# Kernel optimization log

Measured on AMD Instinct MI355X. Metric: run time of the kernel, lower is better.

## Reference

```python
import jax, jax.numpy as jnp
import numpy as np

D_MODEL = 768
N_HEAD = 12
BATCH = 2
SEQ = 2048
MASK_FILL = -100000.0


def setup_inputs() -> dict:
    key = jax.random.key(0)
    ks = jax.random.split(key, 10)
    s = 1.0 / np.sqrt(D_MODEL)
    inp = {
        "xEnc": jax.random.normal(ks[0], (BATCH, SEQ, D_MODEL), jnp.float32),
        "xDec": jax.random.normal(ks[1], (BATCH, SEQ, D_MODEL), jnp.float32),
        # causal mask: True where attention is disallowed (j > i)
        "mask": (jnp.arange(SEQ)[None, :] > jnp.arange(SEQ)[:, None])[None, None, :, :],
        "wQ": jax.random.uniform(ks[2], (D_MODEL, D_MODEL), jnp.float32, -s, s),
        "bQ": jax.random.uniform(ks[3], (D_MODEL,), jnp.float32, -s, s),
        "wK": jax.random.uniform(ks[4], (D_MODEL, D_MODEL), jnp.float32, -s, s),
        "bK": jax.random.uniform(ks[5], (D_MODEL,), jnp.float32, -s, s),
        "wV": jax.random.uniform(ks[6], (D_MODEL, D_MODEL), jnp.float32, -s, s),
        "bV": jax.random.uniform(ks[7], (D_MODEL,), jnp.float32, -s, s),
        "wOut": jax.random.uniform(ks[8], (D_MODEL, D_MODEL), jnp.float32, -s, s),
        "bOut": jax.random.uniform(ks[9], (D_MODEL,), jnp.float32, -s, s),
    }
    return inp


def reference(xEnc, xDec, mask, wQ, bQ, wK, bK, wV, bV, wOut, bOut):
    B, S, D = xEnc.shape
    H = N_HEAD
    Dh = D // H
    # torch Linear: y = x @ W.T + b
    Q = xDec @ wQ.T + bQ
    K = xEnc @ wK.T + bK
    V = xEnc @ wV.T + bV
    Q = Q.reshape(B, S, H, Dh).transpose(0, 2, 1, 3)  # [B,H,S,Dh]
    K = K.reshape(B, S, H, Dh).transpose(0, 2, 1, 3)
    V = V.reshape(B, S, H, Dh).transpose(0, 2, 1, 3)
    score = jnp.einsum("bhqd,bhkd->bhqk", Q, K) / jnp.sqrt(jnp.float32(Dh))
    score = jnp.where(mask, MASK_FILL, score)
    attn = jax.nn.softmax(score, axis=-1)
    ctx = jnp.einsum("bhqk,bhkd->bhqd", attn, V)  # [B,H,S,Dh]
    ctx = ctx.transpose(0, 2, 1, 3).reshape(B, S, D)
    return ctx @ wOut.T + bOut
```

## Files before the change

kernel.cpp:

```cpp
#include <hip/hip_runtime.h>
#include <stdint.h>
#include <stddef.h>

#define DMODEL 768
#define NHEAD 12
#define SEQLEN 2048
#define NBATCH 2
#define DH 64
#define MTOT (NBATCH*SEQLEN)

typedef short s16x4 __attribute__((ext_vector_type(4)));
typedef short s16x8 __attribute__((ext_vector_type(8)));
typedef float f32x4 __attribute__((ext_vector_type(4)));

#define XDECB_OFF 0u
#define XENCB_OFF 3145728u
#define WQB_OFF   6291456u
#define WKB_OFF   6881280u
#define WVB_OFF   7471104u
#define WOUTB_OFF 8060928u
#define QB_OFF    8650752u
#define KB_OFF    11796480u
#define VT_OFF    14942208u
#define CTXB_OFF  18087936u

#define QSCALE 0.18033688011112042f

static __device__ __forceinline__ unsigned short f2bf(float f) {
  union { float f; unsigned int u; } v; v.f = f;
  unsigned int r = v.u + 0x7fffu + ((v.u >> 16) & 1u);
  return (unsigned short)(r >> 16);
}

static __device__ __forceinline__ unsigned int pack2bf(float f0, float f1) {
  union { float f; unsigned int u; } a, b; a.f = f0; b.f = f1;
  return __builtin_amdgcn_perm(b.u + 0x8000u, a.u + 0x8000u, 0x07060302u);
}

#if __has_builtin(__builtin_amdgcn_exp2f)
#define EXP2(x) __builtin_amdgcn_exp2f(x)
#else
#define EXP2(x) exp2f(x)
#endif

static __device__ __forceinline__ f32x4 mfma16(s16x4 a, s16x4 b, f32x4 c) {
  return __builtin_amdgcn_mfma_f32_16x16x16bf16_1k(a, b, c, 0, 0, 0);
}
static __device__ __forceinline__ f32x4 mfma32(s16x8 a, s16x8 b, f32x4 c) {
  return __builtin_amdgcn_mfma_f32_16x16x32_bf16(a, b, c, 0, 0, 0);
}

typedef __attribute__((address_space(3))) unsigned int lds_u32_t;
typedef const __attribute__((address_space(1))) unsigned int glb_u32_t;
static __device__ __forceinline__ void gl_lds16(const unsigned short* g,
                                                unsigned short* l) {
  __builtin_amdgcn_global_load_lds((glb_u32_t*)g, (lds_u32_t*)l, 16, 0, 0);
}

__global__ __launch_bounds__(256) void cvt_kernel(
    const float* __restrict__ xDec, const float* __restrict__ xEnc,
    const float* __restrict__ wQ, const float* __restrict__ wK,
    const float* __restrict__ wV, const float* __restrict__ wOut,
    unsigned short* __restrict__ ws)
{
  const int seg = blockIdx.y;
  const float* src;
  unsigned int n4, off;
  switch (seg) {
    case 0:  src = xDec; n4 = 786432; off = XDECB_OFF; break;
    case 1:  src = xEnc; n4 = 786432; off = XENCB_OFF; break;
    case 2:  src = wQ;   n4 = 147456; off = WQB_OFF;   break;
    case 3:  src = wK;   n4 = 147456; off = WKB_OFF;   break;
    case 4:  src = wV;   n4 = 147456; off = WVB_OFF;   break;
    default: src = wOut; n4 = 147456; off = WOUTB_OFF; break;
  }
  unsigned short* d = ws + off;
  const unsigned int stride = gridDim.x * blockDim.x;
  for (unsigned int i = blockIdx.x * blockDim.x + threadIdx.x; i < n4; i += stride) {
    const float4 v = ((const float4*)src)[i];
    s16x4 p;
    p[0] = (short)f2bf(v.x); p[1] = (short)f2bf(v.y);
    p[2] = (short)f2bf(v.z); p[3] = (short)f2bf(v.w);
    ((s16x4*)d)[i] = p;
  }
}

#define BK 64
#define NKT (DMODEL / BK)

__global__ __launch_bounds__(256, 3) void qkv_gemm(
    const unsigned short* __restrict__ xDecB, const unsigned short* __restrict__ xEncB,
    const unsigned short* __restrict__ wQB, const unsigned short* __restrict__ wKB,
    const unsigned short* __restrict__ wVB,
    const float* __restrict__ bQ, const float* __restrict__ bK, const float* __restrict__ bV,
    unsigned short* __restrict__ Qb, unsigned short* __restrict__ Kb,
    unsigned short* __restrict__ Vt)
{
  const int z = blockIdx.z;
  const unsigned short* __restrict__ A = (z == 0) ? xDecB : xEncB;
  const unsigned short* __restrict__ B = (z == 0) ? wQB : ((z == 1) ? wKB : wVB);
  const float* __restrict__ bias = (z == 0) ? bQ : ((z == 1) ? bK : bV);

  __shared__ unsigned short lA[3][64 * BK];
  __shared__ unsigned short lB[3][64 * BK];

  const int tid  = threadIdx.x;
  const int lane = tid & 63;
  const int wid  = tid >> 6;
  const int ln   = lane & 15;
  const int qd   = lane >> 4;
  const int m0 = blockIdx.x * 64;
  const int n0 = blockIdx.y * 64;
  const int wm = (wid & 1) * 32;
  const int wn = (wid >> 1) * 32;

  int srow[2], scol[2];
  #pragma unroll
  for (int c = 0; c < 2; ++c) {
    const int s = c * 256 + wid * 64 + lane;
    srow[c] = s >> 3;
    scol[c] = (((s & 7) ^ ((s >> 3) & 7)) * 8);
  }

  auto stage = [&](int buf, int k0) {
    #pragma unroll
    for (int c = 0; c < 2; ++c) {
      const int ldsoff = (c * 256 + wid * 64) * 8;
      gl_lds16(A + (size_t)(m0 + srow[c]) * DMODEL + k0 + scol[c], &lA[buf][ldsoff]);
      gl_lds16(B + (size_t)(n0 + srow[c]) * DMODEL + k0 + scol[c], &lB[buf][ldsoff]);
    }
  };

  f32x4 acc[2][2] = {};

  stage(0, 0);
  stage(1, BK);

  auto step = [&](int t, int bc, int bs) {
    if (t == NKT - 1) asm volatile("s_waitcnt vmcnt(0)" ::: "memory");
    else              asm volatile("s_waitcnt vmcnt(4)" ::: "memory");
    __builtin_amdgcn_s_barrier();
    __builtin_amdgcn_sched_barrier(0);
    if (t + 2 < NKT) stage(bs, (t + 2) * BK);
    #pragma unroll
    for (int kc = 0; kc < 2; ++kc) {
      s16x8 af[2], bfr[2];
      #pragma unroll
      for (int i = 0; i < 2; ++i) {
        const int r = wm + i * 16 + ln;
        af[i] = *(const s16x8*)&lA[bc][r * 64 + (((kc * 4 + qd) ^ (r & 7)) * 8)];
      }
      #pragma unroll
      for (int j = 0; j < 2; ++j) {
        const int r = wn + j * 16 + ln;
        bfr[j] = *(const s16x8*)&lB[bc][r * 64 + (((kc * 4 + qd) ^ (r & 7)) * 8)];
      }
      #pragma unroll
      for (int i = 0; i < 2; ++i)
        #pragma unroll
        for (int j = 0; j < 2; ++j)
          acc[i][j] = mfma32(af[i], bfr[j], acc[i][j]);
    }
  };

  for (int tb = 0; tb < NKT; tb += 3) {
    step(tb + 0, 0, 2);
    step(tb + 1, 1, 0);
    step(tb + 2, 2, 1);
  }

  #pragma unroll
  for (int j = 0; j < 2; ++j) {
    const int n_g = n0 + wn + j * 16 + ln;
    const float bv = bias[n_g];
    const int h    = n_g >> 6;
    const int dcol = n_g & 63;
    #pragma unroll
    for (int i = 0; i < 2; ++i) {
      #pragma unroll
      for (int r = 0; r < 4; ++r) {
        const int m_g  = m0 + wm + i * 16 + qd * 4 + r;
        const int bb   = m_g >> 11;
        const int srow2 = m_g & 2047;
        const float val = acc[i][j][r] + bv;
        if (z == 0)
          Qb[((size_t)((bb * NHEAD + h) * SEQLEN + srow2)) * DH + dcol] = f2bf(val * QSCALE);
        else if (z == 1)
          Kb[((size_t)((bb * NHEAD + h) * SEQLEN + srow2)) * DH + dcol] = f2bf(val);
        else
          Vt[((size_t)((bb * NHEAD + h) * DH + dcol)) * SEQLEN + srow2] = f2bf(val);
      }
    }
  }
}

__global__ __launch_bounds__(256, 3) void out_gemm(
    const unsigned short* __restrict__ ctx, const unsigned short* __restrict__ wOutB,
    const float* __restrict__ bOut, float* __restrict__ out)
{
  __shared__ unsigned short lA[3][64 * BK];
  __shared__ unsigned short lB[3][64 * BK];

  const int tid  = threadIdx.x;
  const int lane = tid & 63;
  const int wid  = tid >> 6;
  const int ln   = lane & 15;
  const int qd   = lane >> 4;
  const int m0 = blockIdx.x * 64;
  const int n0 = blockIdx.y * 64;
  const int wm = (wid & 1) * 32;
  const int wn = (wid >> 1) * 32;

  int srow[2], scol[2];
  #pragma unroll
  for (int c = 0; c < 2; ++c) {
    const int s = c * 256 + wid * 64 + lane;
    srow[c] = s >> 3;
    scol[c] = (((s & 7) ^ ((s >> 3) & 7)) * 8);
  }

  auto stage = [&](int buf, int k0) {
    #pragma unroll
    for (int c = 0; c < 2; ++c) {
      const int ldsoff = (c * 256 + wid * 64) * 8;
      gl_lds16(ctx + (size_t)(m0 + srow[c]) * DMODEL + k0 + scol[c], &lA[buf][ldsoff]);
      gl_lds16(wOutB + (size_t)(n0 + srow[c]) * DMODEL + k0 + scol[c], &lB[buf][ldsoff]);
    }
  };

  f32x4 acc[2][2] = {};

  stage(0, 0);
  stage(1, BK);

  auto step = [&](int t, int bc, int bs) {
    if (t == NKT - 1) asm volatile("s_waitcnt vmcnt(0)" ::: "memory");
    else              asm volatile("s_waitcnt vmcnt(4)" ::: "memory");
    __builtin_amdgcn_s_barrier();
    __builtin_amdgcn_sched_barrier(0);
    if (t + 2 < NKT) stage(bs, (t + 2) * BK);
    #pragma unroll
    for (int kc = 0; kc < 2; ++kc) {
      s16x8 af[2], bfr[2];
      #pragma unroll
      for (int i = 0; i < 2; ++i) {
        const int r = wm + i * 16 + ln;
        af[i] = *(const s16x8*)&lA[bc][r * 64 + (((kc * 4 + qd) ^ (r & 7)) * 8)];
      }
      #pragma unroll
      for (int j = 0; j < 2; ++j) {
        const int r = wn + j * 16 + ln;
        bfr[j] = *(const s16x8*)&lB[bc][r * 64 + (((kc * 4 + qd) ^ (r & 7)) * 8)];
      }
      #pragma unroll
      for (int i = 0; i < 2; ++i)
        #pragma unroll
        for (int j = 0; j < 2; ++j)
          acc[i][j] = mfma32(af[i], bfr[j], acc[i][j]);
    }
  };

  for (int tb = 0; tb < NKT; tb += 3) {
    step(tb + 0, 0, 2);
    step(tb + 1, 1, 0);
    step(tb + 2, 2, 1);
  }

  #pragma unroll
  for (int j = 0; j < 2; ++j) {
    const int n_g = n0 + wn + j * 16 + ln;
    const float bv = bOut[n_g];
    #pragma unroll
    for (int i = 0; i < 2; ++i) {
      #pragma unroll
      for (int r = 0; r < 4; ++r) {
        const int m_g = m0 + wm + i * 16 + qd * 4 + r;
        out[(size_t)m_g * DMODEL + n_g] = acc[i][j][r] + bv;
      }
    }
  }
}

#define KVT 128
#define LKP 72
#define LVP 136

__global__ __launch_bounds__(256, 3) void attn_kernel(
    const unsigned short* __restrict__ Qb, const unsigned short* __restrict__ Kb,
    const unsigned short* __restrict__ Vt, unsigned short* __restrict__ ctx,
    float* __restrict__ pout0, float* __restrict__ pout1,
    float* __restrict__ lpart)
{
  __shared__ unsigned short lK[KVT * LKP];
  __shared__ unsigned short lV[DH * LVP];

  const int tid  = threadIdx.x;
  const int lane = tid & 63;
  const int wid  = tid >> 6;
  const int ln   = lane & 15;
  const int qd   = lane >> 4;

  const int ord  = blockIdx.x;
  const int xcd  = ord & 7;
  const int slot = ord >> 3;
  const int bh   = xcd * 3 + (slot >> 5);
  const int p    = slot & 31;

  const bool isA = p < 16;
  const int i  = isA ? p : (p - 16);
  const int Ti = (i + 2) >> 1;

  const unsigned short* Kbase = Kb + (size_t)bh * SEQLEN * DH;
  const unsigned short* Vbase = Vt + (size_t)bh * DH * SEQLEN;
  const int bb = bh / NHEAD;
  const int h  = bh % NHEAD;

  auto run = [&](int q0, int t0, int nt, int mode) {
    const int q_lane = q0 + wid * 16 + ln;
    s16x8 qf[2];
    {
      const unsigned short* Qrow = Qb + ((size_t)bh * SEQLEN + q_lane) * DH;
      qf[0] = *(const s16x8*)(Qrow + qd * 8);
      qf[1] = *(const s16x8*)(Qrow + 32 + qd * 8);
    }
    float l_run = 0.0f;
    f32x4 o_acc[4] = {};

    s16x8 rK[4], rV[4];
    auto load_kv = [&](int kv0) {
      #pragma unroll
      for (int c = 0; c < 4; ++c) {
        const int f = tid + c * 256;
        rK[c] = *(const s16x8*)(Kbase + (size_t)(kv0 + (f >> 3)) * DH + (f & 7) * 8);
      }
      #pragma unroll
      for (int c = 0; c < 4; ++c) {
        const int f = tid + c * 256;
        rV[c] = *(const s16x8*)(Vbase + (size_t)(f >> 4) * SEQLEN + kv0 + (f & 15) * 8);
      }
    };

    load_kv(t0 * KVT);
    for (int t = t0; t < t0 + nt; ++t) {
      const int kv0 = t * KVT;
      #pragma unroll
      for (int c = 0; c < 4; ++c) {
        const int f = tid + c * 256;
        *(s16x8*)&lK[(f >> 3) * LKP + (f & 7) * 8] = rK[c];
      }
      #pragma unroll
      for (int c = 0; c < 4; ++c) {
        const int f = tid + c * 256;
        *(s16x8*)&lV[(f >> 4) * LVP + (f & 15) * 8] = rV[c];
      }
      __syncthreads();
      if (t + 1 < t0 + nt) load_kv(kv0 + KVT);

      f32x4 s_acc[8] = {};
      #pragma unroll
      for (int kc = 0; kc < 2; ++kc) {
        #pragma unroll
        for (int t8 = 0; t8 < 8; ++t8) {
          const s16x8 a = *(const s16x8*)&lK[(t8 * 16 + ln) * LKP + kc * 32 + qd * 8];
          s_acc[t8] = mfma32(a, qf[kc], s_acc[t8]);
        }
      }

      if (kv0 + KVT > q0) {
        #pragma unroll
        for (int t8 = 0; t8 < 8; ++t8) {
          #pragma unroll
          for (int r = 0; r < 4; ++r) {
            const int kv = kv0 + t8 * 16 + qd * 4 + r;
            s_acc[t8][r] = (kv > q_lane) ? -1e30f : s_acc[t8][r];
          }
        }
      }

      s16x4 pf[8];
      #pragma unroll
      for (int t8 = 0; t8 < 8; ++t8) {
        const float p0 = EXP2(s_acc[t8][0]);
        const float p1 = EXP2(s_acc[t8][1]);
        const float p2 = EXP2(s_acc[t8][2]);
        const float p3 = EXP2(s_acc[t8][3]);
        l_run += (p0 + p1) + (p2 + p3);
        union { unsigned int u[2]; s16x4 v; } pk;
        pk.u[0] = pack2bf(p0, p1);
        pk.u[1] = pack2bf(p2, p3);
        pf[t8] = pk.v;
      }

      #pragma unroll
      for (int t8 = 0; t8 < 8; ++t8) {
        #pragma unroll
        for (int j = 0; j < 4; ++j) {
          const s16x4 b = *(const s16x4*)&lV[(j * 16 + ln) * LVP + t8 * 16 + qd * 4];
          o_acc[j] = mfma16(pf[t8], b, o_acc[j]);
        }
      }
      __syncthreads();
    }

    l_run += __shfl_xor(l_run, 16);
    l_run += __shfl_xor(l_run, 32);

    if (mode == 0) {
      #pragma unroll
      for (int r = 0; r < 4; ++r) {
        const float lr  = __shfl(l_run, qd * 4 + r);
        const float inv = 1.0f / lr;
        const int q_g = q0 + wid * 16 + qd * 4 + r;
        unsigned short* dst = ctx + ((size_t)bb * SEQLEN + q_g) * DMODEL + h * DH;
        #pragma unroll
        for (int j = 0; j < 4; ++j)
          dst[j * 16 + ln] = f2bf(o_acc[j][r] * inv);
      }
    } else {
      float* PO = (mode == 1) ? pout1 : pout0;
      float* LO = lpart + ((mode == 1) ? (24 * 1024) : 0);
      const int qbase = q0 - 1024 + wid * 16;
      if (lane < 16)
        LO[bh * 1024 + qbase + lane] = l_run;
      #pragma unroll
      for (int j = 0; j < 4; ++j)
        #pragma unroll
        for (int r = 0; r < 4; ++r)
          PO[((size_t)bh * 1024 + qbase + qd * 4 + r) * 64 + j * 16 + ln] =
              o_acc[j][r];
    }
  };

  if (isA) {
    run(i * 64, 0, Ti, 0);
    run((31 - i) * 64, 0, 9 - Ti, 1);
  } else {
    run((31 - i) * 64, 9 - Ti, 8, 2);
  }
}

__global__ __launch_bounds__(256) void norm_kernel(
    const float* __restrict__ pout0, const float* __restrict__ pout1,
    const float* __restrict__ lpart, unsigned short* __restrict__ ctx)
{
  const int e4  = blockIdx.x * 256 + threadIdx.x;
  const int d4  = e4 & 15;
  const int row = e4 >> 4;
  const int bh  = row >> 10;
  const int qr  = row & 1023;
  const float l = lpart[row] + lpart[24 * 1024 + row];
  const float inv = 1.0f / l;
  const float4 a = ((const float4*)pout0)[e4];
  const float4 b = ((const float4*)pout1)[e4];
  const int bb = bh / NHEAD;
  const int h  = bh % NHEAD;
  unsigned short* dst =
      ctx + ((size_t)bb * SEQLEN + 1024 + qr) * DMODEL + h * DH + d4 * 4;
  s16x4 o;
  o[0] = (short)f2bf((a.x + b.x) * inv);
  o[1] = (short)f2bf((a.y + b.y) * inv);
  o[2] = (short)f2bf((a.z + b.z) * inv);
  o[3] = (short)f2bf((a.w + b.w) * inv);
  *(s16x4*)dst = o;
}

extern "C" void kernel_launch(void* const* d_in, const int* in_sizes, int n_in,
                              void* d_out, int out_size, void* d_ws, size_t ws_size,
                              hipStream_t stream)
{
  const float* xEnc = (const float*)d_in[0];
  const float* xDec = (const float*)d_in[1];
  const float* wQ   = (const float*)d_in[3];
  const float* bQ   = (const float*)d_in[4];
  const float* wK   = (const float*)d_in[5];
  const float* bK   = (const float*)d_in[6];
  const float* wV   = (const float*)d_in[7];
  const float* bV   = (const float*)d_in[8];
  const float* wOut = (const float*)d_in[9];
  const float* bOut = (const float*)d_in[10];

  unsigned short* ws = (unsigned short*)d_ws;
  float* pout0 = (float*)(ws + XDECB_OFF);
  float* pout1 = (float*)(ws + XENCB_OFF);
  float* lpart = (float*)(ws + WQB_OFF);

  cvt_kernel<<<dim3(512, 6), 256, 0, stream>>>(xDec, xEnc, wQ, wK, wV, wOut, ws);
  qkv_gemm<<<dim3(MTOT / 64, DMODEL / 64, 3), 256, 0, stream>>>(
      ws + XDECB_OFF, ws + XENCB_OFF, ws + WQB_OFF, ws + WKB_OFF, ws + WVB_OFF,
      bQ, bK, bV, ws + QB_OFF, ws + KB_OFF, ws + VT_OFF);
  attn_kernel<<<dim3(768), 256, 0, stream>>>(
      ws + QB_OFF, ws + KB_OFF, ws + VT_OFF, ws + CTXB_OFF,
      pout0, pout1, lpart);
  norm_kernel<<<dim3((24 * 1024 * 16) / 256), 256, 0, stream>>>(
      pout0, pout1, lpart, ws + CTXB_OFF);
  out_gemm<<<dim3(MTOT / 64, DMODEL / 64), 256, 0, stream>>>(
      ws + CTXB_OFF, ws + WOUTB_OFF, bOut, (float*)d_out);
}
```

Before: 183.1 us.

## Split KV tile across warps with direct global fragment loads and LDS reduction

The attention kernel no longer stages K/V tiles in shared memory. Each of the four warps now handles all 64 queries for its own 32-key slice of each 128-key tile, loading K and V fragments straight from global memory into registers. Partial outputs and row sums are combined at the end with a two-step tree reduction through shared memory. This removes per-tile LDS staging and barriers, but costs more registers (64 output accumulators), uncoalesced strided global loads without prefetch, and an extra reduction phase.

```diff
diff --git a/kernel.cpp b/kernel.cpp
--- a/kernel.cpp
+++ b/kernel.cpp
@@ -282,8 +282,7 @@
 }
 
 #define KVT 128
-#define LKP 72
-#define LVP 136
+#define RST 68
 
 __global__ __launch_bounds__(256, 3) void attn_kernel(
     const unsigned short* __restrict__ Qb, const unsigned short* __restrict__ Kb,
@@ -291,8 +290,8 @@
     float* __restrict__ pout0, float* __restrict__ pout1,
     float* __restrict__ lpart)
 {
-  __shared__ unsigned short lK[KVT * LKP];
-  __shared__ unsigned short lV[DH * LVP];
+  __shared__ float lO[2][64 * RST];
+  __shared__ float lL[2][64];
 
   const int tid  = threadIdx.x;
   const int lane = tid & 63;
@@ -316,119 +315,171 @@
   const int h  = bh % NHEAD;
 
   auto run = [&](int q0, int t0, int nt, int mode) {
-    const int q_lane = q0 + wid * 16 + ln;
-    s16x8 qf[2];
-    {
-      const unsigned short* Qrow = Qb + ((size_t)bh * SEQLEN + q_lane) * DH;
-      qf[0] = *(const s16x8*)(Qrow + qd * 8);
-      qf[1] = *(const s16x8*)(Qrow + 32 + qd * 8);
-    }
-    float l_run = 0.0f;
-    f32x4 o_acc[4] = {};
-
-    s16x8 rK[4], rV[4];
-    auto load_kv = [&](int kv0) {
-      #pragma unroll
-      for (int c = 0; c < 4; ++c) {
-        const int f = tid + c * 256;
-        rK[c] = *(const s16x8*)(Kbase + (size_t)(kv0 + (f >> 3)) * DH + (f & 7) * 8);
-      }
-      #pragma unroll
-      for (int c = 0; c < 4; ++c) {
-        const int f = tid + c * 256;
-        rV[c] = *(const s16x8*)(Vbase + (size_t)(f >> 4) * SEQLEN + kv0 + (f & 15) * 8);
-      }
-    };
-
-    load_kv(t0 * KVT);
+    s16x8 Qf[4][2];
+    #pragma unroll
+    for (int qc = 0; qc < 4; ++qc)
+      #pragma unroll
+      for (int kc = 0; kc < 2; ++kc)
+        Qf[qc][kc] = *(const s16x8*)(Qb +
+            ((size_t)bh * SEQLEN + q0 + qc * 16 + ln) * DH + kc * 32 + qd * 8);
+
+    float l_acc[4] = {};
+    f32x4 o_acc[4][4] = {};
+
     for (int t = t0; t < t0 + nt; ++t) {
       const int kv0 = t * KVT;
-      #pragma unroll
-      for (int c = 0; c < 4; ++c) {
-        const int f = tid + c * 256;
-        *(s16x8*)&lK[(f >> 3) * LKP + (f & 7) * 8] = rK[c];
-      }
-      #pragma unroll
-      for (int c = 0; c < 4; ++c) {
-        const int f = tid + c * 256;
-        *(s16x8*)&lV[(f >> 4) * LVP + (f & 15) * 8] = rV[c];
-      }
-      __syncthreads();
-      if (t + 1 < t0 + nt) load_kv(kv0 + KVT);
-
-      f32x4 s_acc[8] = {};
-      #pragma unroll
-      for (int kc = 0; kc < 2; ++kc) {
-        #pragma unroll
-        for (int t8 = 0; t8 < 8; ++t8) {
-          const s16x8 a = *(const s16x8*)&lK[(t8 * 16 + ln) * LKP + kc * 32 + qd * 8];
-          s_acc[t8] = mfma32(a, qf[kc], s_acc[t8]);
+      const int kvb = kv0 + wid * 32;
+
+      s16x8 kf8[2][2];
+      #pragma unroll
+      for (int kf = 0; kf < 2; ++kf)
+        #pragma unroll
+        for (int kc = 0; kc < 2; ++kc)
+          kf8[kf][kc] = *(const s16x8*)(Kbase +
+              (size_t)(kvb + kf * 16 + ln) * DH + kc * 32 + qd * 8);
+
+      s16x4 vf4[2][4];
+      #pragma unroll
+      for (int kf = 0; kf < 2; ++kf)
+        #pragma unroll
+        for (int dc = 0; dc < 4; ++dc)
+          vf4[kf][dc] = *(const s16x4*)(Vbase +
+              (size_t)(dc * 16 + ln) * SEQLEN + kvb + kf * 16 + qd * 4);
+
+      const bool diag = (kv0 + KVT > q0);
+      s16x4 pf[2][4];
+      #pragma unroll
+      for (int kf = 0; kf < 2; ++kf) {
+        f32x4 s_acc[4] = {};
+        #pragma unroll
+        for (int qc = 0; qc < 4; ++qc) {
+          s_acc[qc] = mfma32(kf8[kf][0], Qf[qc][0], s_acc[qc]);
+          s_acc[qc] = mfma32(kf8[kf][1], Qf[qc][1], s_acc[qc]);
         }
-      }
-
-      if (kv0 + KVT > q0) {
-        #pragma unroll
-        for (int t8 = 0; t8 < 8; ++t8) {
+        if (diag) {
+          #pragma unroll
+          for (int qc = 0; qc < 4; ++qc)
+            #pragma unroll
+            for (int r = 0; r < 4; ++r) {
+              const int kv = kvb + kf * 16 + qd * 4 + r;
+              const int q  = q0 + qc * 16 + ln;
+              s_acc[qc][r] = (kv > q) ? -1e30f : s_acc[qc][r];
+            }
+        }
+        #pragma unroll
+        for (int qc = 0; qc < 4; ++qc) {
+          const float p0 = EXP2(s_acc[qc][0]);
+          const float p1 = EXP2(s_acc[qc][1]);
+          const float p2 = EXP2(s_acc[qc][2]);
+          const float p3 = EXP2(s_acc[qc][3]);
+          l_acc[qc] += (p0 + p1) + (p2 + p3);
+          union { unsigned int u[2]; s16x4 v; } pk;
+          pk.u[0] = pack2bf(p0, p1);
+          pk.u[1] = pack2bf(p2, p3);
+          pf[kf][qc] = pk.v;
+        }
+      }
+
+      #pragma unroll
+      for (int kf = 0; kf < 2; ++kf)
+        #pragma unroll
+        for (int qc = 0; qc < 4; ++qc)
+          #pragma unroll
+          for (int dc = 0; dc < 4; ++dc)
+            o_acc[qc][dc] = mfma16(pf[kf][qc], vf4[kf][dc], o_acc[qc][dc]);
+    }
+
+    #pragma unroll
+    for (int qc = 0; qc < 4; ++qc) {
+      l_acc[qc] += __shfl_xor(l_acc[qc], 16);
+      l_acc[qc] += __shfl_xor(l_acc[qc], 32);
+    }
+
+    if (wid >= 2) {
+      #pragma unroll
+      for (int qc = 0; qc < 4; ++qc) {
+        lL[wid - 2][qc * 16 + ln] = l_acc[qc];
+        #pragma unroll
+        for (int dc = 0; dc < 4; ++dc)
+          #pragma unroll
+          for (int r = 0; r < 4; ++r)
+            lO[wid - 2][(qc * 16 + qd * 4 + r) * RST + dc * 16 + ln] =
+                o_acc[qc][dc][r];
+      }
+    }
+    __syncthreads();
+    if (wid < 2) {
+      #pragma unroll
+      for (int qc = 0; qc < 4; ++qc) {
+        l_acc[qc] += lL[wid][qc * 16 + ln];
+        #pragma unroll
+        for (int dc = 0; dc < 4; ++dc)
+          #pragma unroll
+          for (int r = 0; r < 4; ++r)
+            o_acc[qc][dc][r] +=
+                lO[wid][(qc * 16 + qd * 4 + r) * RST + dc * 16 + ln];
+      }
+    }
+    __syncthreads();
+    if (wid == 1) {
+      #pragma unroll
+      for (int qc = 0; qc < 4; ++qc) {
+        lL[0][qc * 16 + ln] = l_acc[qc];
+        #pragma unroll
+        for (int dc = 0; dc < 4; ++dc)
+          #pragma unroll
+          for (int r = 0; r < 4; ++r)
+            lO[0][(qc * 16 + qd * 4 + r) * RST + dc * 16 + ln] =
+                o_acc[qc][dc][r];
+      }
+    }
+    __syncthreads();
+    if (wid == 0) {
+      #pragma unroll
+      for (int qc = 0; qc < 4; ++qc) {
+        l_acc[qc] += lL[0][qc * 16 + ln];
+        #pragma unroll
+        for (int dc = 0; dc < 4; ++dc)
+          #pragma unroll
+          for (int r = 0; r < 4; ++r)
+            o_acc[qc][dc][r] +=
+                lO[0][(qc * 16 + qd * 4 + r) * RST + dc * 16 + ln];
+      }
+      if (mode == 0) {
+        #pragma unroll
+        for (int qc = 0; qc < 4; ++qc) {
           #pragma unroll
           for (int r = 0; r < 4; ++r) {
-            const int kv = kv0 + t8 * 16 + qd * 4 + r;
-            s_acc[t8][r] = (kv > q_lane) ? -1e30f : s_acc[t8][r];
+            const float lr  = __shfl(l_acc[qc], qd * 4 + r);
+            const float inv = 1.0f / lr;
+            const int q_g = q0 + qc * 16 + qd * 4 + r;
+            unsigned short* dst =
+                ctx + ((size_t)bb * SEQLEN + q_g) * DMODEL + h * DH;
+            #pragma unroll
+            for (int dc = 0; dc < 4; ++dc)
+              dst[dc * 16 + ln] = f2bf(o_acc[qc][dc][r] * inv);
           }
         }
-      }
-
-      s16x4 pf[8];
-      #pragma unroll
-      for (int t8 = 0; t8 < 8; ++t8) {
-        const float p0 = EXP2(s_acc[t8][0]);
-        const float p1 = EXP2(s_acc[t8][1]);
-        const float p2 = EXP2(s_acc[t8][2]);
-        const float p3 = EXP2(s_acc[t8][3]);
-        l_run += (p0 + p1) + (p2 + p3);
-        union { unsigned int u[2]; s16x4 v; } pk;
-        pk.u[0] = pack2bf(p0, p1);
-        pk.u[1] = pack2bf(p2, p3);
-        pf[t8] = pk.v;
-      }
-
-      #pragma unroll
-      for (int t8 = 0; t8 < 8; ++t8) {
-        #pragma unroll
-        for (int j = 0; j < 4; ++j) {
-          const s16x4 b = *(const s16x4*)&lV[(j * 16 + ln) * LVP + t8 * 16 + qd * 4];
-          o_acc[j] = mfma16(pf[t8], b, o_acc[j]);
+      } else {
+        float* PO = (mode == 1) ? pout1 : pout0;
+        float* LO = lpart + ((mode == 1) ? (24 * 1024) : 0);
+        const int qbase = q0 - 1024;
+        if (lane < 16) {
+          #pragma unroll
+          for (int qc = 0; qc < 4; ++qc)
+            LO[bh * 1024 + qbase + qc * 16 + lane] = l_acc[qc];
         }
-      }
-      __syncthreads();
-    }
-
-    l_run += __shfl_xor(l_run, 16);
-    l_run += __shfl_xor(l_run, 32);
-
-    if (mode == 0) {
-      #pragma unroll
-      for (int r = 0; r < 4; ++r) {
-        const float lr  = __shfl(l_run, qd * 4 + r);
-        const float inv = 1.0f / lr;
-        const int q_g = q0 + wid * 16 + qd * 4 + r;
-        unsigned short* dst = ctx + ((size_t)bb * SEQLEN + q_g) * DMODEL + h * DH;
-        #pragma unroll
-        for (int j = 0; j < 4; ++j)
-          dst[j * 16 + ln] = f2bf(o_acc[j][r] * inv);
-      }
-    } else {
-      float* PO = (mode == 1) ? pout1 : pout0;
-      float* LO = lpart + ((mode == 1) ? (24 * 1024) : 0);
-      const int qbase = q0 - 1024 + wid * 16;
-      if (lane < 16)
-        LO[bh * 1024 + qbase + lane] = l_run;
-      #pragma unroll
-      for (int j = 0; j < 4; ++j)
-        #pragma unroll
-        for (int r = 0; r < 4; ++r)
-          PO[((size_t)bh * 1024 + qbase + qd * 4 + r) * 64 + j * 16 + ln] =
-              o_acc[j][r];
-    }
+        #pragma unroll
+        for (int qc = 0; qc < 4; ++qc)
+          #pragma unroll
+          for (int dc = 0; dc < 4; ++dc)
+            #pragma unroll
+            for (int r = 0; r < 4; ++r)
+              PO[((size_t)bh * 1024 + qbase + qc * 16 + qd * 4 + r) * 64 +
+                 dc * 16 + ln] = o_acc[qc][dc][r];
+      }
+    }
+    __syncthreads();
   };
 
   if (isA) {
```

New measurement: 204.1 us. 11.5% more time.

## Restructure attention into 2x2 warp split with async double-buffered LDS loads

Applied to the files above, without the earlier changes.

Rewrites the attention kernel so K/V tiles are staged directly from global memory into double-buffered, XOR-swizzled LDS through gl_lds16, replacing the register-staged copy with padded rows. Warps are split two ways over queries and two ways over the KV tile, so each warp computes 32 queries against 64 keys and reuses each K/V fragment for two query chunks. The two KV-half partial outputs and row sums are reduced through LDS at the end. Occupancy drops from 3 to 2 blocks per CU because LDS use is larger, and the end-of-run reduction adds extra barriers.

```diff
diff --git a/kernel.cpp b/kernel.cpp
--- a/kernel.cpp
+++ b/kernel.cpp
@@ -282,23 +282,23 @@
 }
 
 #define KVT 128
-#define LKP 72
-#define LVP 136
-
-__global__ __launch_bounds__(256, 3) void attn_kernel(
+#define RST 68
+
+__global__ __launch_bounds__(256, 2) void attn_kernel(
     const unsigned short* __restrict__ Qb, const unsigned short* __restrict__ Kb,
     const unsigned short* __restrict__ Vt, unsigned short* __restrict__ ctx,
     float* __restrict__ pout0, float* __restrict__ pout1,
     float* __restrict__ lpart)
 {
-  __shared__ unsigned short lK[KVT * LKP];
-  __shared__ unsigned short lV[DH * LVP];
+  __shared__ __attribute__((aligned(16))) unsigned short smem[2][16384];
 
   const int tid  = threadIdx.x;
   const int lane = tid & 63;
   const int wid  = tid >> 6;
   const int ln   = lane & 15;
   const int qd   = lane >> 4;
+  const int qw   = wid & 1;
+  const int kw   = wid >> 1;
 
   const int ord  = blockIdx.x;
   const int xcd  = ord & 7;
@@ -315,120 +315,162 @@
   const int bb = bh / NHEAD;
   const int h  = bh % NHEAD;
 
+  float* rO = (float*)&smem[0][0];
+  float* rL = rO + 64 * RST;
+
+  auto stage = [&](int b, int kv0) {
+    #pragma unroll
+    for (int c = 0; c < 4; ++c) {
+      const int f = tid + c * 256;
+      gl_lds16(Kbase + (size_t)(kv0 + (f >> 3)) * DH + ((f & 7) ^ ((f >> 3) & 7)) * 8,
+               &smem[b][f * 8]);
+    }
+    #pragma unroll
+    for (int c = 0; c < 4; ++c) {
+      const int f = tid + c * 256;
+      gl_lds16(Vbase + (size_t)(f >> 4) * SEQLEN + kv0 + ((f & 15) ^ ((f >> 4) & 15)) * 8,
+               &smem[b][8192 + f * 8]);
+    }
+  };
+
   auto run = [&](int q0, int t0, int nt, int mode) {
-    const int q_lane = q0 + wid * 16 + ln;
-    s16x8 qf[2];
-    {
-      const unsigned short* Qrow = Qb + ((size_t)bh * SEQLEN + q_lane) * DH;
-      qf[0] = *(const s16x8*)(Qrow + qd * 8);
-      qf[1] = *(const s16x8*)(Qrow + 32 + qd * 8);
-    }
-    float l_run = 0.0f;
-    f32x4 o_acc[4] = {};
-
-    s16x8 rK[4], rV[4];
-    auto load_kv = [&](int kv0) {
-      #pragma unroll
-      for (int c = 0; c < 4; ++c) {
-        const int f = tid + c * 256;
-        rK[c] = *(const s16x8*)(Kbase + (size_t)(kv0 + (f >> 3)) * DH + (f & 7) * 8);
-      }
-      #pragma unroll
-      for (int c = 0; c < 4; ++c) {
-        const int f = tid + c * 256;
-        rV[c] = *(const s16x8*)(Vbase + (size_t)(f >> 4) * SEQLEN + kv0 + (f & 15) * 8);
-      }
-    };
-
-    load_kv(t0 * KVT);
+    s16x8 Qf[2][2];
+    #pragma unroll
+    for (int qc = 0; qc < 2; ++qc)
+      #pragma unroll
+      for (int kc = 0; kc < 2; ++kc)
+        Qf[qc][kc] = *(const s16x8*)(Qb +
+            ((size_t)bh * SEQLEN + q0 + qw * 32 + qc * 16 + ln) * DH + kc * 32 + qd * 8);
+
+    float l_acc[2] = {};
+    f32x4 acc[2][4] = {};
+
+    stage(0, t0 * KVT);
     for (int t = t0; t < t0 + nt; ++t) {
+      const int b = (t - t0) & 1;
+      asm volatile("s_waitcnt vmcnt(0)" ::: "memory");
+      __builtin_amdgcn_s_barrier();
+      __builtin_amdgcn_sched_barrier(0);
+      if (t + 1 < t0 + nt) stage(b ^ 1, (t + 1) * KVT);
+
+      const unsigned short* lK = &smem[b][0];
+      const unsigned short* lV = &smem[b][8192];
       const int kv0 = t * KVT;
-      #pragma unroll
-      for (int c = 0; c < 4; ++c) {
-        const int f = tid + c * 256;
-        *(s16x8*)&lK[(f >> 3) * LKP + (f & 7) * 8] = rK[c];
-      }
-      #pragma unroll
-      for (int c = 0; c < 4; ++c) {
-        const int f = tid + c * 256;
-        *(s16x8*)&lV[(f >> 4) * LVP + (f & 15) * 8] = rV[c];
-      }
-      __syncthreads();
-      if (t + 1 < t0 + nt) load_kv(kv0 + KVT);
-
-      f32x4 s_acc[8] = {};
-      #pragma unroll
-      for (int kc = 0; kc < 2; ++kc) {
-        #pragma unroll
-        for (int t8 = 0; t8 < 8; ++t8) {
-          const s16x8 a = *(const s16x8*)&lK[(t8 * 16 + ln) * LKP + kc * 32 + qd * 8];
-          s_acc[t8] = mfma32(a, qf[kc], s_acc[t8]);
+      const bool diag = (kv0 + KVT > q0);
+
+      s16x4 pf[4][2];
+      #pragma unroll
+      for (int t8 = 0; t8 < 4; ++t8) {
+        const int row = kw * 64 + t8 * 16 + ln;
+        const s16x8 k0 = *(const s16x8*)&lK[row * 64 + ((qd ^ (ln & 7)) * 8)];
+        const s16x8 k1 = *(const s16x8*)&lK[row * 64 + (((4 + qd) ^ (ln & 7)) * 8)];
+        f32x4 sq[2] = {};
+        sq[0] = mfma32(k0, Qf[0][0], sq[0]);
+        sq[0] = mfma32(k1, Qf[0][1], sq[0]);
+        sq[1] = mfma32(k0, Qf[1][0], sq[1]);
+        sq[1] = mfma32(k1, Qf[1][1], sq[1]);
+        #pragma unroll
+        for (int qc = 0; qc < 2; ++qc) {
+          if (diag) {
+            #pragma unroll
+            for (int r = 0; r < 4; ++r) {
+              const int kv = kv0 + kw * 64 + t8 * 16 + qd * 4 + r;
+              const int q  = q0 + qw * 32 + qc * 16 + ln;
+              sq[qc][r] = (kv > q) ? -1e30f : sq[qc][r];
+            }
+          }
+          const float p0 = EXP2(sq[qc][0]);
+          const float p1 = EXP2(sq[qc][1]);
+          const float p2 = EXP2(sq[qc][2]);
+          const float p3 = EXP2(sq[qc][3]);
+          l_acc[qc] += (p0 + p1) + (p2 + p3);
+          union { unsigned int u[2]; s16x4 v; } pk;
+          pk.u[0] = pack2bf(p0, p1);
+          pk.u[1] = pack2bf(p2, p3);
+          pf[t8][qc] = pk.v;
         }
       }
 
-      if (kv0 + KVT > q0) {
-        #pragma unroll
-        for (int t8 = 0; t8 < 8; ++t8) {
+      #pragma unroll
+      for (int t8 = 0; t8 < 4; ++t8) {
+        #pragma unroll
+        for (int dc = 0; dc < 4; ++dc) {
+          const int vrow  = dc * 16 + ln;
+          const int slotv = (kw * 8 + 2 * t8 + (qd >> 1)) ^ ln;
+          const s16x4 bv = *(const s16x4*)&lV[vrow * 128 + slotv * 8 + (qd & 1) * 4];
+          acc[0][dc] = mfma16(pf[t8][0], bv, acc[0][dc]);
+          acc[1][dc] = mfma16(pf[t8][1], bv, acc[1][dc]);
+        }
+      }
+    }
+    __syncthreads();
+
+    #pragma unroll
+    for (int qc = 0; qc < 2; ++qc) {
+      l_acc[qc] += __shfl_xor(l_acc[qc], 16);
+      l_acc[qc] += __shfl_xor(l_acc[qc], 32);
+    }
+
+    if (kw == 1) {
+      if (lane < 16) {
+        rL[qw * 32 + lane]      = l_acc[0];
+        rL[qw * 32 + 16 + lane] = l_acc[1];
+      }
+      #pragma unroll
+      for (int qc = 0; qc < 2; ++qc)
+        #pragma unroll
+        for (int dc = 0; dc < 4; ++dc)
+          #pragma unroll
+          for (int r = 0; r < 4; ++r)
+            rO[(qw * 32 + qc * 16 + qd * 4 + r) * RST + dc * 16 + ln] =
+                acc[qc][dc][r];
+    }
+    __syncthreads();
+    if (kw == 0) {
+      #pragma unroll
+      for (int qc = 0; qc < 2; ++qc) {
+        l_acc[qc] += rL[qw * 32 + qc * 16 + ln];
+        #pragma unroll
+        for (int dc = 0; dc < 4; ++dc)
+          #pragma unroll
+          for (int r = 0; r < 4; ++r)
+            acc[qc][dc][r] +=
+                rO[(qw * 32 + qc * 16 + qd * 4 + r) * RST + dc * 16 + ln];
+      }
+      if (mode == 0) {
+        #pragma unroll
+        for (int qc = 0; qc < 2; ++qc) {
           #pragma unroll
           for (int r = 0; r < 4; ++r) {
-            const int kv = kv0 + t8 * 16 + qd * 4 + r;
-            s_acc[t8][r] = (kv > q_lane) ? -1e30f : s_acc[t8][r];
+            const float lr  = __shfl(l_acc[qc], qd * 4 + r);
+            const float inv = 1.0f / lr;
+            const int q_g = q0 + qw * 32 + qc * 16 + qd * 4 + r;
+            unsigned short* dst =
+                ctx + ((size_t)bb * SEQLEN + q_g) * DMODEL + h * DH;
+            #pragma unroll
+            for (int dc = 0; dc < 4; ++dc)
+              dst[dc * 16 + ln] = f2bf(acc[qc][dc][r] * inv);
           }
         }
-      }
-
-      s16x4 pf[8];
-      #pragma unroll
-      for (int t8 = 0; t8 < 8; ++t8) {
-        const float p0 = EXP2(s_acc[t8][0]);
-        const float p1 = EXP2(s_acc[t8][1]);
-        const float p2 = EXP2(s_acc[t8][2]);
-        const float p3 = EXP2(s_acc[t8][3]);
-        l_run += (p0 + p1) + (p2 + p3);
-        union { unsigned int u[2]; s16x4 v; } pk;
-        pk.u[0] = pack2bf(p0, p1);
-        pk.u[1] = pack2bf(p2, p3);
-        pf[t8] = pk.v;
-      }
-
-      #pragma unroll
-      for (int t8 = 0; t8 < 8; ++t8) {
-        #pragma unroll
-        for (int j = 0; j < 4; ++j) {
-          const s16x4 b = *(const s16x4*)&lV[(j * 16 + ln) * LVP + t8 * 16 + qd * 4];
-          o_acc[j] = mfma16(pf[t8], b, o_acc[j]);
+      } else {
+        float* PO = (mode == 1) ? pout1 : pout0;
+        float* LO = lpart + ((mode == 1) ? (24 * 1024) : 0);
+        const int qbase = q0 - 1024 + qw * 32;
+        if (lane < 16) {
+          LO[bh * 1024 + qbase + lane]      = l_acc[0];
+          LO[bh * 1024 + qbase + 16 + lane] = l_acc[1];
         }
-      }
-      __syncthreads();
-    }
-
-    l_run += __shfl_xor(l_run, 16);
-    l_run += __shfl_xor(l_run, 32);
-
-    if (mode == 0) {
-      #pragma unroll
-      for (int r = 0; r < 4; ++r) {
-        const float lr  = __shfl(l_run, qd * 4 + r);
-        const float inv = 1.0f / lr;
-        const int q_g = q0 + wid * 16 + qd * 4 + r;
-        unsigned short* dst = ctx + ((size_t)bb * SEQLEN + q_g) * DMODEL + h * DH;
-        #pragma unroll
-        for (int j = 0; j < 4; ++j)
-          dst[j * 16 + ln] = f2bf(o_acc[j][r] * inv);
-      }
-    } else {
-      float* PO = (mode == 1) ? pout1 : pout0;
-      float* LO = lpart + ((mode == 1) ? (24 * 1024) : 0);
-      const int qbase = q0 - 1024 + wid * 16;
-      if (lane < 16)
-        LO[bh * 1024 + qbase + lane] = l_run;
-      #pragma unroll
-      for (int j = 0; j < 4; ++j)
-        #pragma unroll
-        for (int r = 0; r < 4; ++r)
-          PO[((size_t)bh * 1024 + qbase + qd * 4 + r) * 64 + j * 16 + ln] =
-              o_acc[j][r];
-    }
+        #pragma unroll
+        for (int qc = 0; qc < 2; ++qc)
+          #pragma unroll
+          for (int dc = 0; dc < 4; ++dc)
+            #pragma unroll
+            for (int r = 0; r < 4; ++r)
+              PO[((size_t)bh * 1024 + qbase + qc * 16 + qd * 4 + r) * 64 +
+                 dc * 16 + ln] = acc[qc][dc][r];
+      }
+    }
+    __syncthreads();
   };
 
   if (isA) {
```

New measurement: 178.3 us. 1.03x faster.
